# Kernel optimization log

Measured on AMD Instinct MI355X. Metric: run time of the kernel, lower is better.

## Reference

```python
import jax, jax.numpy as jnp
import numpy as np

EPS_WN = 1e-6
EPS_BN = 1e-5

def wn_linear(x, W):
    # WeightNormlinear with scale=False, bias=False: y = (x W^T) / ||W_row||
    norm = jnp.sqrt(jnp.sum(W * W, axis=1) + EPS_WN)  # [out]
    return (x @ W.T) / norm

def hyper_weights(z, W0, W2, W3):
    # z: [N_O, N_I, E] -> conv weight [N_O*16, N_I*16, 3, 3], bias [N_O*16]
    N_O, N_I, E = z.shape
    bias = wn_linear(z.reshape(N_O, N_I * E), W0).reshape(-1)      # [N_O*16]
    w = wn_linear(z, W2).reshape(N_O, N_I, 16, E)                  # fc2
    w = wn_linear(w, W3)                                           # fc3 -> [N_O,N_I,16,16*9]
    w = w.reshape(N_O, N_I, 16, 16, 3, 3).transpose(0, 2, 1, 3, 4, 5)
    w = w.reshape(N_O * 16, N_I * 16, 3, 3)
    return jnp.sign(w), jnp.sign(bias)  # BinarizeWF forward

def conv3x3(x, w, stride):
    return jax.lax.conv_general_dilated(
        x, w, (stride, stride), ((1, 1), (1, 1)),
        dimension_numbers=('NCHW', 'OIHW', 'NCHW'))

def batchnorm(x, gamma, beta):
    # training-mode BN: biased batch statistics over (N,H,W)
    mean = jnp.mean(x, axis=(0, 2, 3), keepdims=True)
    var = jnp.var(x, axis=(0, 2, 3), keepdims=True)
    return gamma[None, :, None, None] * (x - mean) * jax.lax.rsqrt(var + EPS_BN) + beta[None, :, None, None]

def setup_inputs() -> dict:
    key = jax.random.key(0)
    ks = jax.random.split(key, 10)
    B, C, H, W = 16, 256, 56, 56
    E = 64
    NO = NI = C // 16
    def uni(k, shape, s):
        return jax.random.uniform(k, shape, jnp.float32, -s, s)
    stdv_z = 5.0 / np.sqrt(E)          # random_z init
    stdv0 = 4.0 / np.sqrt(E * NI)      # fc0: in = E*N_I
    stdv23 = 4.0 / np.sqrt(E)          # fc2/fc3: in = E
    return {
        'x': jax.random.normal(ks[0], (B, C, H, W), jnp.float32),
        'z1': uni(ks[1], (NO, NI, E), stdv_z),
        'W0_1': uni(ks[2], (16, E * NI), stdv0),
        'W2_1': uni(ks[3], (16 * E, E), stdv23),
        'W3_1': uni(ks[4], (16 * 9, E), stdv23),
        'gamma1': jnp.ones((C,), jnp.float32),
        'beta1': jnp.zeros((C,), jnp.float32),
        'z2': uni(ks[5], (NO, NO, E), stdv_z),
        'W0_2': uni(ks[6], (16, E * NO), stdv0),
        'W2_2': uni(ks[7], (16 * E, E), stdv23),
        'W3_2': uni(ks[8], (16 * 9, E), stdv23),
        'gamma2': jnp.ones((C,), jnp.float32),
        'beta2': jnp.zeros((C,), jnp.float32),
    }

def reference(x, z1, W0_1, W2_1, W3_1, gamma1, beta1,
              z2, W0_2, W2_2, W3_2, gamma2, beta2):
    residual = x
    # conv1 (stride=1): binarize activations (C != 3), hyper-generated binary weights
    w1, b1 = hyper_weights(z1, W0_1, W2_1, W3_1)
    out = conv3x3(jnp.sign(x), w1, 1) + b1[None, :, None, None]
    out = batchnorm(out, gamma1, beta1)
    # conv2
    w2, b2 = hyper_weights(z2, W0_2, W2_2, W3_2)
    out2 = conv3x3(jnp.sign(out), w2, 1) + b2[None, :, None, None]
    out2 = batchnorm(out2, gamma2, beta2)
    return out2 + residual
```

## Files before the change

### kernel.cpp

```cpp
#include <hip/hip_runtime.h>
#include <stdint.h>

typedef int v4i __attribute__((ext_vector_type(4)));
typedef int v16i __attribute__((ext_vector_type(16)));



__global__ __launch_bounds__(256, 2) void hyper_kernel(
    const float* __restrict__ z1, const float* __restrict__ W21,
    const float* __restrict__ W31, const float* __restrict__ z2,
    const float* __restrict__ W22, const float* __restrict__ W32,
    int8_t* __restrict__ Wb1, int8_t* __restrict__ Wb2,
    const float* __restrict__ W01, const float* __restrict__ W02,
    int* __restrict__ b1, int* __restrict__ b2,
    unsigned long long* __restrict__ sums) {
  __shared__ __align__(16) float Wt[16384];
  __shared__ __align__(16) float hbuf[1024];
  __shared__ __align__(16) float zsh[64];
  __shared__ __align__(16) int8_t pk[2304];
  const int tid = threadIdx.x;

  if (blockIdx.x >= 512) {
    const int pb = blockIdx.x - 512;
    if (pb == 32) {
      #pragma unroll
      for (int i = 0; i < 4; ++i) sums[i * 256 + tid] = 0ull;
      return;
    }
    float* zs = Wt;
    const int set = pb >> 4, o = pb & 15;
    const float* z = set ? z2 : z1;
    const float* W0 = set ? W02 : W01;
    int* bout = set ? b2 : b1;
    #pragma unroll
    for (int i = 0; i < 4; ++i) zs[i * 256 + tid] = z[(size_t)o * 1024 + i * 256 + tid];
    __syncthreads();
    const int j = tid >> 4, l = tid & 15;
    const float* wr = W0 + (size_t)j * 1024;
    double acc = 0.0;
    #pragma unroll 4
    for (int it = 0; it < 16; ++it) {
      float4 w4 = *(const float4*)&wr[it * 64 + l * 4];
      float4 z4 = *(const float4*)&zs[it * 64 + l * 4];
      acc += (double)w4.x * z4.x + (double)w4.y * z4.y + (double)w4.z * z4.z + (double)w4.w * z4.w;
    }
    #pragma unroll
    for (int m = 1; m < 16; m <<= 1) acc += __shfl_xor(acc, m, 64);
    if (l == 0) bout[o * 16 + j] = (acc > 0.0) ? 1 : ((acc < 0.0) ? -1 : 0);
    return;
  }

  const int set = blockIdx.x >> 8;
  const int oi = blockIdx.x & 255;
  const float* z = set ? z2 : z1;
  const float* W2 = set ? W22 : W21;
  const float* W3 = set ? W32 : W31;
  int8_t* Wb = set ? Wb2 : Wb1;

  if (tid < 16) *(float4*)&zsh[tid * 4] = ((const float4*)(z + (size_t)oi * 64))[tid];
  __syncthreads();

  for (int c = 0; c < 4; ++c) {
    if (c) __syncthreads();
    const float4* src = (const float4*)W2 + c * 4096;
    #pragma unroll
    for (int i = 0; i < 16; ++i) {
      int G = i * 256 + tid;
      int row = G >> 4, g = G & 15;
      *(float4*)&Wt[row * 64 + ((g ^ (row & 15)) << 2)] = src[G];
    }
    __syncthreads();
    double ax = 0, ay = 0, az = 0, aw = 0;
    double nx = 0, ny = 0, nz = 0, nw = 0;
    #pragma unroll
    for (int it = 0; it < 16; ++it) {
      float4 w4 = *(const float4*)&Wt[tid * 64 + ((it ^ (tid & 15)) << 2)];
      float4 z4 = *(const float4*)&zsh[it * 4];
      ax += (double)w4.x * z4.x; ay += (double)w4.y * z4.y;
      az += (double)w4.z * z4.z; aw += (double)w4.w * z4.w;
      nx += (double)w4.x * w4.x; ny += (double)w4.y * w4.y;
      nz += (double)w4.z * w4.z; nw += (double)w4.w * w4.w;
    }
    double dot = (ax + ay) + (az + aw);
    double ss = (nx + ny) + (nz + nw);
    hbuf[c * 256 + tid] = (float)(dot / sqrt(ss + 1e-6));
  }
  __syncthreads();

  {
    const float4* src = (const float4*)W3;
    #pragma unroll
    for (int i = 0; i < 9; ++i) {
      int G = i * 256 + tid;
      int row = G >> 4, g = G & 15;
      *(float4*)&Wt[row * 64 + ((g ^ (row & 15)) << 2)] = src[G];
    }
  }
  __syncthreads();

  {
    const int q = tid >> 4, sub = tid & 15;
    #pragma unroll
    for (int k = 0; k < 9; ++k) {
      int jj = sub + (k << 4);
      double ax = 0, ay = 0, az = 0, aw = 0;
      #pragma unroll
      for (int it = 0; it < 16; ++it) {
        float4 w4 = *(const float4*)&Wt[jj * 64 + ((it ^ sub) << 2)];
        float4 h4 = *(const float4*)&hbuf[q * 64 + it * 4];
        ax += (double)w4.x * h4.x; ay += (double)w4.y * h4.y;
        az += (double)w4.z * h4.z; aw += (double)w4.w * h4.w;
      }
      double acc = (ax + ay) + (az + aw);
      int8_t sgn = (acc > 0.0) ? (int8_t)1 : ((acc < 0.0) ? (int8_t)(-1) : (int8_t)0);
      int tp = jj / 9, tap = jj - tp * 9;
      pk[tap * 256 + q * 16 + tp] = sgn;
    }
  }
  __syncthreads();

  if (tid < 144) {
    const int tap = tid >> 4, qq = tid & 15;
    const int o = oi >> 4, ii = oi & 15;
    const int chunk = ((tap << 2) + (ii >> 2)) * 2 + ((ii >> 1) & 1);
    v4i val = *(const v4i*)&pk[tap * 256 + qq * 16];
    *(v4i*)(Wb + (size_t)chunk * 8192 + (size_t)(o * 16 + qq) * 32 + ((ii & 1) << 4)) = val;
  }
}


__global__ void signx_kernel(const float* __restrict__ x, int8_t* __restrict__ Sp) {
  const int tid = threadIdx.x;
  const int f = blockIdx.x + 58 * blockIdx.y;
  const int orig = (f & 7) * 116 + (f >> 3);
  const int b = orig / 58, h = orig % 58;
  int8_t* rowp = Sp + ((size_t)b * 58 + h) * 58 * 256;
  if (h == 0 || h == 57) {
    #pragma unroll
    for (int i = 0; i < 4; ++i) {
      int idx = i * 256 + tid;
      if (idx < 928) *(v4i*)(rowp + (size_t)idx * 16) = (v4i){0, 0, 0, 0};
    }
    return;
  }
  __shared__ int8_t t[56 * 256];
  const float* xb = x + (size_t)b * 802816 + (size_t)(h - 1) * 56;
  for (int i = 0; i < 56; ++i) {
    int flat = i * 256 + tid;
    int c = flat / 56, w = flat - c * 56;
    float v = xb[(size_t)c * 3136 + w];
    t[w * 256 + (c ^ ((w & 31) << 3))] = (v > 0.f) ? 1 : ((v < 0.f) ? -1 : 0);
  }
  if (tid < 32) {
    int col = tid >> 4;
    *(v4i*)(rowp + (col ? 57 * 256 : 0) + (tid & 15) * 16) = (v4i){0, 0, 0, 0};
  }
  __syncthreads();
  int8_t* dst = rowp + 256;
  for (int i = 0; i < 7; ++i) {
    int f8 = i * 256 + tid;
    int w = f8 >> 5, c0 = (f8 & 31) << 3;
    uint2 v = *(const uint2*)&t[w * 256 + (c0 ^ ((w & 31) << 3))];
    *(uint2*)(dst + (size_t)w * 256 + c0) = v;
  }
}


template <int MODE>
__global__ __launch_bounds__(512, 4) void conv_kernel(
    const int8_t* __restrict__ Sp, const int16_t* __restrict__ rawin,
    const float* __restrict__ par, const int8_t* __restrict__ WbP,
    const int* __restrict__ bias, int16_t* __restrict__ raw,
    unsigned long long* __restrict__ sums)
{
  __shared__ __align__(16) int8_t lds[59392];
  const int tid = threadIdx.x;
  const int lane = tid & 63;
  const int f0 = blockIdx.x + 28 * blockIdx.y;
  const int orig = (f0 & 7) * 56 + (f0 >> 3);
  const int b = orig / 28, bx = orig % 28;
  const int H0 = bx << 1;

  const int n = lane & 31, kg = lane >> 5;
  const int wid = tid >> 6;
  const int cogrp = wid & 3, pxgrp = wid >> 2;

  const int8_t* Abase = WbP + (size_t)((cogrp << 6) + n) * 32 + (kg << 4);
  v4i Ar[2][2][2];
  #pragma unroll
  for (int c2 = 0; c2 < 2; ++c2)
    #pragma unroll
    for (int a = 0; a < 2; ++a)
      Ar[0][c2][a] = *(const v4i*)(Abase + (size_t)c2 * 8192 + a * 1024);

  if (MODE == 0) {
    const int8_t* SpB = Sp + ((size_t)b * 58 + H0) * 58 * 256;
    #pragma unroll
    for (int ph = 0; ph < 2; ++ph) {
      v4i tmp[4];
      #pragma unroll
      for (int it = 0; it < 4; ++it) {
        int G = (ph * 4 + it) * 512 + tid;
        if (G < 3712) {
          int pp = G >> 4, gl = G & 15;
          int wp = pp % 58;
          tmp[it] = *(const v4i*)(SpB + pp * 256 + ((gl ^ (wp & 7)) << 4));
        }
      }
      #pragma unroll
      for (int it = 0; it < 4; ++it) {
        int G = (ph * 4 + it) * 512 + tid;
        if (G < 3712) *(v4i*)(lds + (G << 4)) = tmp[it];
      }
    }
  } else {
    const int gsrc = tid & 15;
    const int ppt = tid >> 4;
    float thr[16]; int sf[16];
    const float* thrp = par + 768;
    const int* sfp = (const int*)(par + 1024);
    #pragma unroll
    for (int j = 0; j < 16; ++j) { thr[j] = thrp[gsrc * 16 + j]; sf[j] = sfp[gsrc * 16 + j]; }
    #pragma unroll
    for (int it = 0; it < 8; ++it) {
      int pp = it * 32 + ppt;
      if (pp < 232) {
        int prow = pp / 58, pcol = pp - prow * 58;
        int ir = H0 + prow - 1, ic = pcol - 1;
        v4i outv = (v4i){0, 0, 0, 0};
        if (ir >= 0 && ir <= 55 && ic >= 0 && ic <= 55) {
          const int16_t* src = rawin + ((size_t)(b * 3136 + ir * 56 + ic)) * 256 + gsrc * 16;
          v4i lo = *(const v4i*)src;
          v4i hi = *(const v4i*)(src + 8);
          #pragma unroll
          for (int j = 0; j < 16; ++j) {
            int wd = (j < 8) ? lo[(j >> 1) & 3] : hi[(j >> 1) & 3];
            int v = (j & 1) ? (wd >> 16) : (int)(short)wd;
            float fv = (float)v;
            int bj = (fv > thr[j]) ? sf[j] : ((fv < thr[j]) ? -sf[j] : 0);
            outv[j >> 2] |= (bj & 0xff) << ((j & 3) << 3);
          }
        }
        *(v4i*)(lds + ((pp << 4) + (gsrc ^ (pcol & 7))) * 16) = outv;
      }
    }
  }

  int pixoff[2], wcol[2];
  #pragma unroll
  for (int f = 0; f < 2; ++f) {
    int px = (((pxgrp << 1) + f) << 5) + n;
    if (px > 111) px = 111;
    int hh = px / 56, ww = px - hh * 56;
    pixoff[f] = hh * 58 + ww;
    wcol[f] = ww;
  }

  v16i acc[2][2];
  #pragma unroll
  for (int f = 0; f < 2; ++f)
    #pragma unroll
    for (int a = 0; a < 2; ++a)
      #pragma unroll
      for (int e = 0; e < 16; ++e) acc[f][a][e] = 0;

  __syncthreads();

  #pragma unroll
  for (int ks = 0; ks < 36; ++ks) {
    const int cur = ks & 1;
    if (ks + 1 < 36) {
      #pragma unroll
      for (int c2 = 0; c2 < 2; ++c2)
        #pragma unroll
        for (int a = 0; a < 2; ++a)
          Ar[cur ^ 1][c2][a] = *(const v4i*)(Abase + (size_t)((ks + 1) * 2 + c2) * 8192 + a * 1024);
    }
    const int tap = ks >> 2, c64 = ks & 3;
    const int r = tap / 3, s = tap - 3 * (tap / 3);
    #pragma unroll
    for (int c2 = 0; c2 < 2; ++c2) {
      v4i Af0 = Ar[cur][c2][0], Af1 = Ar[cur][c2][1];
      #pragma unroll
      for (int f = 0; f < 2; ++f) {
        const int gb = (c64 << 2) + (c2 << 1) + kg;
        v4i Bf = *(const v4i*)(lds + ((pixoff[f] + r * 58 + s) << 8)
                               + ((gb ^ ((wcol[f] + s) & 7)) << 4));
        acc[f][0] = __builtin_amdgcn_mfma_i32_32x32x32_i8(Af0, Bf, acc[f][0], 0, 0, 0);
        acc[f][1] = __builtin_amdgcn_mfma_i32_32x32x32_i8(Af1, Bf, acc[f][1], 0, 0, 0);
      }
    }
  }

  __syncthreads();
  #pragma unroll
  for (int f = 0; f < 2; ++f) {
    int px = (((pxgrp << 1) + f) << 5) + n;
    if (px < 112) {
      #pragma unroll
      for (int a = 0; a < 2; ++a) {
        #pragma unroll
        for (int q = 0; q < 4; ++q) {
          int co = (cogrp << 6) + (a << 5) + (q << 3) + (kg << 2);
          v4i bi = *(const v4i*)(bias + co);
          short4 o;
          o.x = (short)(acc[f][a][q * 4 + 0] + bi.x);
          o.y = (short)(acc[f][a][q * 4 + 1] + bi.y);
          o.z = (short)(acc[f][a][q * 4 + 2] + bi.z);
          o.w = (short)(acc[f][a][q * 4 + 3] + bi.w);
          int g = co >> 3;
          *(short4*)(lds + px * 512 + ((g ^ (px & 31)) << 4) + (kg << 3)) = o;
        }
      }
    }
  }
  __syncthreads();
  const int pbase = b * 3136 + bx * 112;
  const int gg = tid & 31;
  int s8[8], q8[8];
  #pragma unroll
  for (int j = 0; j < 8; ++j) { s8[j] = 0; q8[j] = 0; }
  #pragma unroll
  for (int i = 0; i < 7; ++i) {
    int rrow = i * 16 + (tid >> 5);
    v4i val = *(const v4i*)(lds + rrow * 512 + ((gg ^ (rrow & 31)) << 4));
    *(v4i*)(raw + (size_t)(pbase + rrow) * 256 + gg * 8) = val;
    #pragma unroll
    for (int j = 0; j < 8; ++j) {
      int wd = val[j >> 1];
      int v = (j & 1) ? (wd >> 16) : (int)(short)wd;
      s8[j] += v; q8[j] += v * v;
    }
  }
  __syncthreads();
  int* red = (int*)lds;
  #pragma unroll
  for (int j = 0; j < 8; ++j) { red[tid * 8 + j] = s8[j]; red[4096 + tid * 8 + j] = q8[j]; }
  __syncthreads();
  if (tid < 256) {
    const int ch = tid;
    const int own = ch >> 3, sub = ch & 7;
    long long S = 0, Q = 0;
    #pragma unroll
    for (int jj = 0; jj < 16; ++jj) {
      int t2 = own + 32 * jj;
      S += red[t2 * 8 + sub];
      Q += red[4096 + t2 * 8 + sub];
    }
    atomicAdd(&sums[ch], (unsigned long long)S);
    atomicAdd(&sums[256 + ch], (unsigned long long)Q);
  }
}


__global__ void finalize_kernel(const unsigned long long* __restrict__ sums,
                                const float* __restrict__ gamma, const float* __restrict__ beta,
                                float* __restrict__ par) {
  const int c = threadIdx.x;
  double S = (double)(long long)sums[c];
  double Q = (double)(long long)sums[256 + c];
  double mean = S / 50176.0;
  double var = Q / 50176.0 - mean * mean;
  double istd = 1.0 / sqrt(var + 1e-5);
  double A = (double)gamma[c] * istd;
  float Af = (float)A;
  par[c] = (float)mean;
  par[256 + c] = Af;
  par[512 + c] = beta[c];
  float thr; int sf;
  if (Af > 0.f)      { thr = (float)(mean - (double)beta[c] / A); sf = 1; }
  else if (Af < 0.f) { thr = (float)(mean - (double)beta[c] / A); sf = -1; }
  else               { thr = -1e30f; sf = (beta[c] > 0.f) ? 1 : ((beta[c] < 0.f) ? -1 : 0); }
  par[768 + c] = thr;
  ((int*)par)[1024 + c] = sf;
}


__global__ void final_kernel(const int16_t* __restrict__ raw2, const float* __restrict__ par,
                             const float* __restrict__ x, float* __restrict__ out) {
  __shared__ float t[256 * 57];
  const int tid = threadIdx.x;
  const int f0 = blockIdx.x + 56 * blockIdx.y;
  const int orig = (f0 & 7) * 112 + (f0 >> 3);
  const int b = orig / 56, h = orig % 56;
  const int rowp = b * 3136 + h * 56;
  for (int i = 0; i < 7; ++i) {
    int f8 = i * 256 + tid;
    int px = f8 >> 5, c0 = (f8 & 31) << 3;
    float m[8], A[8], bb[8];
    *(float4*)&m[0]  = *(const float4*)&par[c0];
    *(float4*)&m[4]  = *(const float4*)&par[c0 + 4];
    *(float4*)&A[0]  = *(const float4*)&par[256 + c0];
    *(float4*)&A[4]  = *(const float4*)&par[256 + c0 + 4];
    *(float4*)&bb[0] = *(const float4*)&par[512 + c0];
    *(float4*)&bb[4] = *(const float4*)&par[512 + c0 + 4];
    v4i vv = *(const v4i*)(raw2 + (size_t)(rowp + px) * 256 + c0);
    #pragma unroll
    for (int j = 0; j < 8; ++j) {
      int wd = vv[j >> 1];
      int v = (j & 1) ? (wd >> 16) : (int)(short)wd;
      t[(c0 + j) * 57 + px] = ((float)v - m[j]) * A[j] + bb[j];
    }
  }
  __syncthreads();
  const float* xb = x + (size_t)b * 802816 + (size_t)h * 56;
  float* ob = out + (size_t)b * 802816 + (size_t)h * 56;
  for (int i = 0; i < 16; ++i) {
    int idx = i * 256 + tid;
    int c = idx >> 4, wq = idx & 15;
    if (wq < 14) {
      int w0 = wq * 4;
      float4 xv = *(const float4*)(xb + (size_t)c * 3136 + w0);
      float4 o;
      o.x = t[c * 57 + w0 + 0] + xv.x;
      o.y = t[c * 57 + w0 + 1] + xv.y;
      o.z = t[c * 57 + w0 + 2] + xv.z;
      o.w = t[c * 57 + w0 + 3] + xv.w;
      *(float4*)(ob + (size_t)c * 3136 + w0) = o;
    }
  }
}


extern "C" void kernel_launch(void* const* d_in, const int* in_sizes, int n_in,
                              void* d_out, int out_size, void* d_ws, size_t ws_size,
                              hipStream_t stream) {
  const float* x      = (const float*)d_in[0];
  const float* z1     = (const float*)d_in[1];
  const float* W0_1   = (const float*)d_in[2];
  const float* W2_1   = (const float*)d_in[3];
  const float* W3_1   = (const float*)d_in[4];
  const float* gamma1 = (const float*)d_in[5];
  const float* beta1  = (const float*)d_in[6];
  const float* z2     = (const float*)d_in[7];
  const float* W0_2   = (const float*)d_in[8];
  const float* W2_2   = (const float*)d_in[9];
  const float* W3_2   = (const float*)d_in[10];
  const float* gamma2 = (const float*)d_in[11];
  const float* beta2  = (const float*)d_in[12];
  float* out = (float*)d_out;

  char* ws = (char*)d_ws;
  size_t off = 0;
  auto alloc = [&](size_t sz) -> void* {
    void* p = ws + off;
    off += (sz + 255) & ~(size_t)255;
    return p;
  };
  int8_t* Sp1   = (int8_t*)alloc(13778944);
  int16_t* raw1 = (int16_t*)alloc(25690112);
  int16_t* raw2 = (int16_t*)alloc(25690112);
  int8_t* Wb1   = (int8_t*)alloc(589824);
  int8_t* Wb2   = (int8_t*)alloc(589824);
  int* b1       = (int*)alloc(1024);
  int* b2       = (int*)alloc(1024);
  unsigned long long* sums = (unsigned long long*)alloc(8192);
  float* par1   = (float*)alloc(5120);
  float* par2   = (float*)alloc(5120);
  if (ws_size < off) return;

  hyper_kernel<<<545, 256, 0, stream>>>(z1, W2_1, W3_1, z2, W2_2, W3_2, Wb1, Wb2,
                                        W0_1, W0_2, b1, b2, sums);
  signx_kernel<<<dim3(58, 16), 256, 0, stream>>>(x, Sp1);
  conv_kernel<0><<<dim3(28, 16), 512, 0, stream>>>(Sp1, nullptr, nullptr, Wb1, b1, raw1, sums);
  finalize_kernel<<<1, 256, 0, stream>>>(sums, gamma1, beta1, par1);
  conv_kernel<1><<<dim3(28, 16), 512, 0, stream>>>(nullptr, raw1, par1, Wb2, b2, raw2, sums + 512);
  finalize_kernel<<<1, 256, 0, stream>>>(sums + 512, gamma2, beta2, par2);
  final_kernel<<<dim3(56, 16), 256, 0, stream>>>(raw2, par2, x, out);
}
```

Baseline: 180.7 us.

## Fuse sign-pack into hyper kernel and fold BN finalize into consumers

Merges the sign/pad packing of x into the hyper-weight kernel as extra blocks, so both independent preprocessing steps run in one launch. Removes the two single-block finalize kernels by recomputing the BN mean/istd/threshold per block inside conv_kernel<1> and final_kernel. This cuts the launch count from seven to four. In exchange, every consumer block redundantly does 256 double-precision stat computations, and the fused kernel carries hyper_kernel's large LDS footprint, which may limit occupancy of the sign-pack blocks.

```diff
diff --git a/kernel.cpp b/kernel.cpp
--- a/kernel.cpp
+++ b/kernel.cpp
@@ -6,19 +6,57 @@
 
 
 
-__global__ __launch_bounds__(256, 2) void hyper_kernel(
+__global__ __launch_bounds__(256, 2) void fused_pre_kernel(
     const float* __restrict__ z1, const float* __restrict__ W21,
     const float* __restrict__ W31, const float* __restrict__ z2,
     const float* __restrict__ W22, const float* __restrict__ W32,
     int8_t* __restrict__ Wb1, int8_t* __restrict__ Wb2,
     const float* __restrict__ W01, const float* __restrict__ W02,
     int* __restrict__ b1, int* __restrict__ b2,
-    unsigned long long* __restrict__ sums) {
+    unsigned long long* __restrict__ sums,
+    const float* __restrict__ x, int8_t* __restrict__ Sp) {
   __shared__ __align__(16) float Wt[16384];
   __shared__ __align__(16) float hbuf[1024];
   __shared__ __align__(16) float zsh[64];
   __shared__ __align__(16) int8_t pk[2304];
   const int tid = threadIdx.x;
+
+  if (blockIdx.x >= 545) {
+    const int fs = blockIdx.x - 545;
+    const int xcd = blockIdx.x & 7;
+    const int orig = xcd * 116 + (fs >> 3);
+    const int b = orig / 58, h = orig % 58;
+    int8_t* rowp = Sp + ((size_t)b * 58 + h) * 58 * 256;
+    if (h == 0 || h == 57) {
+      #pragma unroll
+      for (int i = 0; i < 4; ++i) {
+        int idx = i * 256 + tid;
+        if (idx < 928) *(v4i*)(rowp + (size_t)idx * 16) = (v4i){0, 0, 0, 0};
+      }
+      return;
+    }
+    int8_t* t = (int8_t*)Wt;
+    const float* xb = x + (size_t)b * 802816 + (size_t)(h - 1) * 56;
+    for (int i = 0; i < 56; ++i) {
+      int flat = i * 256 + tid;
+      int c = flat / 56, w = flat - c * 56;
+      float v = xb[(size_t)c * 3136 + w];
+      t[w * 256 + (c ^ ((w & 31) << 3))] = (v > 0.f) ? 1 : ((v < 0.f) ? -1 : 0);
+    }
+    if (tid < 32) {
+      int col = tid >> 4;
+      *(v4i*)(rowp + (col ? 57 * 256 : 0) + (tid & 15) * 16) = (v4i){0, 0, 0, 0};
+    }
+    __syncthreads();
+    int8_t* dst = rowp + 256;
+    for (int i = 0; i < 7; ++i) {
+      int f8 = i * 256 + tid;
+      int w = f8 >> 5, c0 = (f8 & 31) << 3;
+      uint2 v = *(const uint2*)&t[w * 256 + (c0 ^ ((w & 31) << 3))];
+      *(uint2*)(dst + (size_t)w * 256 + c0) = v;
+    }
+    return;
+  }
 
   if (blockIdx.x >= 512) {
     const int pb = blockIdx.x - 512;
@@ -129,51 +167,17 @@
 }
 
 
-__global__ void signx_kernel(const float* __restrict__ x, int8_t* __restrict__ Sp) {
-  const int tid = threadIdx.x;
-  const int f = blockIdx.x + 58 * blockIdx.y;
-  const int orig = (f & 7) * 116 + (f >> 3);
-  const int b = orig / 58, h = orig % 58;
-  int8_t* rowp = Sp + ((size_t)b * 58 + h) * 58 * 256;
-  if (h == 0 || h == 57) {
-    #pragma unroll
-    for (int i = 0; i < 4; ++i) {
-      int idx = i * 256 + tid;
-      if (idx < 928) *(v4i*)(rowp + (size_t)idx * 16) = (v4i){0, 0, 0, 0};
-    }
-    return;
-  }
-  __shared__ int8_t t[56 * 256];
-  const float* xb = x + (size_t)b * 802816 + (size_t)(h - 1) * 56;
-  for (int i = 0; i < 56; ++i) {
-    int flat = i * 256 + tid;
-    int c = flat / 56, w = flat - c * 56;
-    float v = xb[(size_t)c * 3136 + w];
-    t[w * 256 + (c ^ ((w & 31) << 3))] = (v > 0.f) ? 1 : ((v < 0.f) ? -1 : 0);
-  }
-  if (tid < 32) {
-    int col = tid >> 4;
-    *(v4i*)(rowp + (col ? 57 * 256 : 0) + (tid & 15) * 16) = (v4i){0, 0, 0, 0};
-  }
-  __syncthreads();
-  int8_t* dst = rowp + 256;
-  for (int i = 0; i < 7; ++i) {
-    int f8 = i * 256 + tid;
-    int w = f8 >> 5, c0 = (f8 & 31) << 3;
-    uint2 v = *(const uint2*)&t[w * 256 + (c0 ^ ((w & 31) << 3))];
-    *(uint2*)(dst + (size_t)w * 256 + c0) = v;
-  }
-}
-
-
 template <int MODE>
 __global__ __launch_bounds__(512, 4) void conv_kernel(
     const int8_t* __restrict__ Sp, const int16_t* __restrict__ rawin,
-    const float* __restrict__ par, const int8_t* __restrict__ WbP,
-    const int* __restrict__ bias, int16_t* __restrict__ raw,
-    unsigned long long* __restrict__ sums)
+    const unsigned long long* __restrict__ sumsIn,
+    const float* __restrict__ gamma, const float* __restrict__ beta,
+    const int8_t* __restrict__ WbP, const int* __restrict__ bias,
+    int16_t* __restrict__ raw, unsigned long long* __restrict__ sumsOut)
 {
   __shared__ __align__(16) int8_t lds[59392];
+  __shared__ float thrS[256];
+  __shared__ int sfS[256];
   const int tid = threadIdx.x;
   const int lane = tid & 63;
   const int f0 = blockIdx.x + 28 * blockIdx.y;
@@ -184,6 +188,24 @@
   const int n = lane & 31, kg = lane >> 5;
   const int wid = tid >> 6;
   const int cogrp = wid & 3, pxgrp = wid >> 2;
+
+  if (MODE == 1) {
+    if (tid < 256) {
+      double S = (double)(long long)sumsIn[tid];
+      double Q = (double)(long long)sumsIn[256 + tid];
+      double mean = S / 50176.0;
+      double var = Q / 50176.0 - mean * mean;
+      double istd = 1.0 / sqrt(var + 1e-5);
+      double A = (double)gamma[tid] * istd;
+      float Af = (float)A;
+      float thr; int sf;
+      if (Af > 0.f)      { thr = (float)(mean - (double)beta[tid] / A); sf = 1; }
+      else if (Af < 0.f) { thr = (float)(mean - (double)beta[tid] / A); sf = -1; }
+      else               { thr = -1e30f; sf = (beta[tid] > 0.f) ? 1 : ((beta[tid] < 0.f) ? -1 : 0); }
+      thrS[tid] = thr; sfS[tid] = sf;
+    }
+    __syncthreads();
+  }
 
   const int8_t* Abase = WbP + (size_t)((cogrp << 6) + n) * 32 + (kg << 4);
   v4i Ar[2][2][2];
@@ -217,10 +239,8 @@
     const int gsrc = tid & 15;
     const int ppt = tid >> 4;
     float thr[16]; int sf[16];
-    const float* thrp = par + 768;
-    const int* sfp = (const int*)(par + 1024);
-    #pragma unroll
-    for (int j = 0; j < 16; ++j) { thr[j] = thrp[gsrc * 16 + j]; sf[j] = sfp[gsrc * 16 + j]; }
+    #pragma unroll
+    for (int j = 0; j < 16; ++j) { thr[j] = thrS[gsrc * 16 + j]; sf[j] = sfS[gsrc * 16 + j]; }
     #pragma unroll
     for (int it = 0; it < 8; ++it) {
       int pp = it * 32 + ppt;
@@ -347,53 +367,44 @@
       S += red[t2 * 8 + sub];
       Q += red[4096 + t2 * 8 + sub];
     }
-    atomicAdd(&sums[ch], (unsigned long long)S);
-    atomicAdd(&sums[256 + ch], (unsigned long long)Q);
+    atomicAdd(&sumsOut[ch], (unsigned long long)S);
+    atomicAdd(&sumsOut[256 + ch], (unsigned long long)Q);
   }
 }
 
 
-__global__ void finalize_kernel(const unsigned long long* __restrict__ sums,
-                                const float* __restrict__ gamma, const float* __restrict__ beta,
-                                float* __restrict__ par) {
-  const int c = threadIdx.x;
-  double S = (double)(long long)sums[c];
-  double Q = (double)(long long)sums[256 + c];
-  double mean = S / 50176.0;
-  double var = Q / 50176.0 - mean * mean;
-  double istd = 1.0 / sqrt(var + 1e-5);
-  double A = (double)gamma[c] * istd;
-  float Af = (float)A;
-  par[c] = (float)mean;
-  par[256 + c] = Af;
-  par[512 + c] = beta[c];
-  float thr; int sf;
-  if (Af > 0.f)      { thr = (float)(mean - (double)beta[c] / A); sf = 1; }
-  else if (Af < 0.f) { thr = (float)(mean - (double)beta[c] / A); sf = -1; }
-  else               { thr = -1e30f; sf = (beta[c] > 0.f) ? 1 : ((beta[c] < 0.f) ? -1 : 0); }
-  par[768 + c] = thr;
-  ((int*)par)[1024 + c] = sf;
-}
-
-
-__global__ void final_kernel(const int16_t* __restrict__ raw2, const float* __restrict__ par,
+__global__ void final_kernel(const int16_t* __restrict__ raw2,
+                             const unsigned long long* __restrict__ sums2,
+                             const float* __restrict__ gamma, const float* __restrict__ beta,
                              const float* __restrict__ x, float* __restrict__ out) {
   __shared__ float t[256 * 57];
+  __shared__ __align__(16) float mS[256], AS[256], bS[256];
   const int tid = threadIdx.x;
   const int f0 = blockIdx.x + 56 * blockIdx.y;
   const int orig = (f0 & 7) * 112 + (f0 >> 3);
   const int b = orig / 56, h = orig % 56;
   const int rowp = b * 3136 + h * 56;
+  {
+    double S = (double)(long long)sums2[tid];
+    double Q = (double)(long long)sums2[256 + tid];
+    double mean = S / 50176.0;
+    double var = Q / 50176.0 - mean * mean;
+    double istd = 1.0 / sqrt(var + 1e-5);
+    mS[tid] = (float)mean;
+    AS[tid] = gamma[tid] * (float)istd;
+    bS[tid] = beta[tid];
+  }
+  __syncthreads();
   for (int i = 0; i < 7; ++i) {
     int f8 = i * 256 + tid;
     int px = f8 >> 5, c0 = (f8 & 31) << 3;
     float m[8], A[8], bb[8];
-    *(float4*)&m[0]  = *(const float4*)&par[c0];
-    *(float4*)&m[4]  = *(const float4*)&par[c0 + 4];
-    *(float4*)&A[0]  = *(const float4*)&par[256 + c0];
-    *(float4*)&A[4]  = *(const float4*)&par[256 + c0 + 4];
-    *(float4*)&bb[0] = *(const float4*)&par[512 + c0];
-    *(float4*)&bb[4] = *(const float4*)&par[512 + c0 + 4];
+    *(float4*)&m[0]  = *(const float4*)&mS[c0];
+    *(float4*)&m[4]  = *(const float4*)&mS[c0 + 4];
+    *(float4*)&A[0]  = *(const float4*)&AS[c0];
+    *(float4*)&A[4]  = *(const float4*)&AS[c0 + 4];
+    *(float4*)&bb[0] = *(const float4*)&bS[c0];
+    *(float4*)&bb[4] = *(const float4*)&bS[c0 + 4];
     v4i vv = *(const v4i*)(raw2 + (size_t)(rowp + px) * 256 + c0);
     #pragma unroll
     for (int j = 0; j < 8; ++j) {
@@ -455,16 +466,13 @@
   int* b1       = (int*)alloc(1024);
   int* b2       = (int*)alloc(1024);
   unsigned long long* sums = (unsigned long long*)alloc(8192);
-  float* par1   = (float*)alloc(5120);
-  float* par2   = (float*)alloc(5120);
   if (ws_size < off) return;
 
-  hyper_kernel<<<545, 256, 0, stream>>>(z1, W2_1, W3_1, z2, W2_2, W3_2, Wb1, Wb2,
-                                        W0_1, W0_2, b1, b2, sums);
-  signx_kernel<<<dim3(58, 16), 256, 0, stream>>>(x, Sp1);
-  conv_kernel<0><<<dim3(28, 16), 512, 0, stream>>>(Sp1, nullptr, nullptr, Wb1, b1, raw1, sums);
-  finalize_kernel<<<1, 256, 0, stream>>>(sums, gamma1, beta1, par1);
-  conv_kernel<1><<<dim3(28, 16), 512, 0, stream>>>(nullptr, raw1, par1, Wb2, b2, raw2, sums + 512);
-  finalize_kernel<<<1, 256, 0, stream>>>(sums + 512, gamma2, beta2, par2);
-  final_kernel<<<dim3(56, 16), 256, 0, stream>>>(raw2, par2, x, out);
+  fused_pre_kernel<<<1473, 256, 0, stream>>>(z1, W2_1, W3_1, z2, W2_2, W3_2, Wb1, Wb2,
+                                             W0_1, W0_2, b1, b2, sums, x, Sp1);
+  conv_kernel<0><<<dim3(28, 16), 512, 0, stream>>>(Sp1, nullptr, nullptr, nullptr, nullptr,
+                                                   Wb1, b1, raw1, sums);
+  conv_kernel<1><<<dim3(28, 16), 512, 0, stream>>>(nullptr, raw1, sums, gamma1, beta1,
+                                                   Wb2, b2, raw2, sums + 512);
+  final_kernel<<<dim3(56, 16), 256, 0, stream>>>(raw2, sums + 512, gamma2, beta2, x, out);
 }
```

New measurement: 172.8 us. 1.05x faster.
